# Kernel tuning notes

Measured on AMD Instinct MI355X. Metric: run time of the kernel, lower is better.

The kernel has to match this reference:

```python
import jax, jax.numpy as jnp
import numpy as np
import math

B, L, H, D, S, R = 2, 1024, 8, 64, 10, 128


def setup_inputs() -> dict:
    key = jax.random.key(0)
    k1, k2, k3, k4, k5, k6 = jax.random.split(key, 6)
    return {
        "queries": jax.random.normal(k1, (B, L, H, D), jnp.float32),
        "keys": jax.random.normal(k2, (B, L, H, D), jnp.float32),
        "freqs": jax.random.normal(k3, (H, D, S), jnp.float32),
        "offsets": jax.random.normal(k4, (H, D, S), jnp.float32),
        "gains": jax.random.normal(k5, (H, D, S), jnp.float32),
        "z": jax.random.normal(k6, (B, H, D, 2 * S, R), jnp.float32),
    }


def reference(queries, keys, freqs, offsets, gains, z):
    length = queries.shape[1]
    idx = jnp.arange(length, dtype=queries.dtype)  # [L]
    fr = jax.nn.sigmoid(freqs) / 2.0  # [H,D,S]
    two_pi = 2.0 * math.pi
    # phases: [H,D,L,S]
    phases_q = two_pi * fr[:, :, None, :] * idx[None, None, :, None] + offsets[:, :, None, :]
    phases_k = two_pi * fr[:, :, None, :] * idx[None, None, :, None]
    # interleave cos/sin along last dim -> [H,D,L,2S]
    omega_q = jnp.stack([jnp.cos(phases_q), jnp.sin(phases_q)], axis=-1).reshape(
        phases_q.shape[0], phases_q.shape[1], length, 2 * phases_q.shape[-1])
    omega_k = jnp.stack([jnp.cos(phases_k), jnp.sin(phases_k)], axis=-1).reshape(
        phases_k.shape[0], phases_k.shape[1], length, 2 * phases_k.shape[-1])
    # gains: softplus then repeat(1,1,2) -> concat copies along last dim [H,D,2S]
    g = jax.nn.softplus(gains)
    g2 = jnp.concatenate([g, g], axis=-1)
    scale = 1.0 / math.sqrt(z.shape[-1] * queries.shape[-1])  # 1/sqrt(R*D)
    zs = z * (g2[None, :, :, :, None] * scale)  # [B,H,D,2S,R]
    # fused: qbar[b,h,d,l,r] = sum_s omega_q[h,d,l,s] * zs[b,h,d,s,r];
    # qhat[b,l,h,r] = sum_d qbar[b,l,h,d,r] * queries[b,l,h,d]
    qhat = jnp.einsum('hdls,bhdsr,blhd->blhr', omega_q, zs, queries)
    khat = jnp.einsum('hdls,bhdsr,blhd->blhr', omega_k, zs, keys)
    return (qhat, khat)
```

## Files before the change

### kernel.cpp

```cpp
#include <hip/hip_runtime.h>
#include <math.h>


typedef short bf16x8 __attribute__((ext_vector_type(8)));
typedef float f32x16 __attribute__((ext_vector_type(16)));

__device__ __forceinline__ unsigned int rnd_bf16(float x) {
    union { float f; unsigned int u; } v; v.f = x;
    return v.u + 0x8000u;
}
__device__ __forceinline__ unsigned int pack_bf16(float c, float s) {
    return __builtin_amdgcn_perm(rnd_bf16(s), rnd_bf16(c), 0x07060302u);
}

__global__ __launch_bounds__(256) void prep_z(
    const float* __restrict__ freqs, const float* __restrict__ offsets,
    const float* __restrict__ gains, const float* __restrict__ z,
    uint4* __restrict__ zt, float2* __restrict__ frof)
{
    const float scale = 0.011048543456039806f;
    int bid = blockIdx.x;
    int bh = bid / 20, kb = bid - bh * 20;
    int h = bh & 7;
    int dh = (kb >= 10) ? 1 : 0, s = kb - dh * 10;
    int t = threadIdx.x;

    __shared__ float gsl[64];

    if (t < 16) {
        int i = bid * 16 + t;
        int hh = i / 640, rem = i - hh * 640;
        int ss = rem >> 6, dd = rem & 63;
        int src = (hh * 64 + dd) * 10 + ss;
        float fr = 0.5f / (1.0f + __expf(-freqs[src]));
        frof[i] = make_float2(fr, offsets[src] * 0.15915494309189535f);
        frof[5120 + i] = make_float2(fr, 0.0f);
    }
    if (t < 64) {
        int dl = t >> 1, par = t & 1;
        int tt = 2 * s + par;
        int jm = (tt < 10) ? tt : tt - 10;
        float gn = gains[(h * 64 + dh * 32 + dl) * 10 + jm];
        gsl[t] = (fmaxf(gn, 0.0f) + log1pf(__expf(-fabsf(gn)))) * scale;
    }
    __syncthreads();

    const float* zb = z + (size_t)bh * 163840;
    uint4* outb = zt + (size_t)bid * 1024;

    #pragma unroll
    for (int i = 0; i < 4; i++) {
        int e = i * 256 + t;
        int r = (e >> 1) & 127, c8 = e & 1;
        int dl0 = i * 8 + c8 * 4;
        unsigned int u[4];
        #pragma unroll
        for (int m = 0; m < 4; m++) {
            int dl = dl0 + m;
            int d = dh * 32 + dl;
            float ve = zb[((size_t)d * 20 + 2 * s) * 128 + r] * gsl[dl * 2];
            float vo = zb[((size_t)d * 20 + 2 * s + 1) * 128 + r] * gsl[dl * 2 + 1];
            u[m] = pack_bf16(ve, vo);
        }
        outb[e] = make_uint4(u[0], u[1], u[2], u[3]);
    }
}

__global__ __launch_bounds__(256, 4) void spe_gemm(
    const float* __restrict__ queries, const float* __restrict__ keys,
    const float2* __restrict__ frof, const unsigned short* __restrict__ zt,
    float* __restrict__ out)
{
    __shared__ unsigned int At[2][1024];

    int bid = blockIdx.x;
    int h = bid & 7;
    int u = bid >> 3;
    int qk = u & 1, b = (u >> 1) & 1, lt = u >> 2;
    int l0 = lt * 32;

    int t = threadIdx.x, w = t >> 6, lane = t & 63;
    int ml = lane & 31, hi = lane >> 5;
    int arow = t >> 3, pg = t & 7;

    const float* qsrc = (qk ? keys : queries)
                      + ((size_t)(b * 1024 + l0 + arow) * 8 + h) * 64 + pg * 4;
    const float2* fob = frof + qk * 5120 + h * 640 + pg * 4;
    const unsigned short* bbase = zt + (size_t)(b * 8 + h) * 163840
                                + (w * 32 + ml) * 16 + hi * 8;
    float lf = (float)(l0 + arow);
    unsigned int awz = arow * 32 + ((pg ^ (arow & 7)) << 2);

    float4 qf = *(const float4*)(qsrc);

    bf16x8 n0 = *(const bf16x8*)(bbase);
    bf16x8 n1 = *(const bf16x8*)(bbase + 2048);
    bf16x8 n2 = *(const bf16x8*)(bbase + 4096);
    bf16x8 n3 = *(const bf16x8*)(bbase + 6144);
    {
        const float4* fp = (const float4*)(fob);
        float4 fA = fp[0], fB = fp[1];
        float p0 = __builtin_amdgcn_fractf(fmaf(fA.x, lf, fA.y));
        float p1 = __builtin_amdgcn_fractf(fmaf(fA.z, lf, fA.w));
        float p2 = __builtin_amdgcn_fractf(fmaf(fB.x, lf, fB.y));
        float p3 = __builtin_amdgcn_fractf(fmaf(fB.z, lf, fB.w));
        uint4 a4;
        a4.x = pack_bf16(__builtin_amdgcn_cosf(p0) * qf.x, __builtin_amdgcn_sinf(p0) * qf.x);
        a4.y = pack_bf16(__builtin_amdgcn_cosf(p1) * qf.y, __builtin_amdgcn_sinf(p1) * qf.y);
        a4.z = pack_bf16(__builtin_amdgcn_cosf(p2) * qf.z, __builtin_amdgcn_sinf(p2) * qf.z);
        a4.w = pack_bf16(__builtin_amdgcn_cosf(p3) * qf.w, __builtin_amdgcn_sinf(p3) * qf.w);
        *(uint4*)&At[0][awz] = a4;
    }

    f32x16 acc = {};

    #pragma unroll 2
    for (int kb = 0; kb < 20; kb++) {
        __syncthreads();
        int cur = kb & 1;

        bf16x8 c0 = n0, c1 = n1, c2 = n2, c3 = n3;

        int kn = (kb < 19) ? kb + 1 : 19;
        const unsigned short* tp = bbase + (size_t)kn * 8192;
        n0 = *(const bf16x8*)(tp);
        n1 = *(const bf16x8*)(tp + 2048);
        n2 = *(const bf16x8*)(tp + 4096);
        n3 = *(const bf16x8*)(tp + 6144);

        {
            int dh = (kn >= 10) ? 1 : 0;
            int s = kn - dh * 10;
            if (kn == 10) qf = *(const float4*)(qsrc + 32);
            const float4* fp = (const float4*)(fob + s * 64 + dh * 32);
            float4 fA = fp[0], fB = fp[1];
            float p0 = __builtin_amdgcn_fractf(fmaf(fA.x, lf, fA.y));
            float p1 = __builtin_amdgcn_fractf(fmaf(fA.z, lf, fA.w));
            float p2 = __builtin_amdgcn_fractf(fmaf(fB.x, lf, fB.y));
            float p3 = __builtin_amdgcn_fractf(fmaf(fB.z, lf, fB.w));
            uint4 a4;
            a4.x = pack_bf16(__builtin_amdgcn_cosf(p0) * qf.x, __builtin_amdgcn_sinf(p0) * qf.x);
            a4.y = pack_bf16(__builtin_amdgcn_cosf(p1) * qf.y, __builtin_amdgcn_sinf(p1) * qf.y);
            a4.z = pack_bf16(__builtin_amdgcn_cosf(p2) * qf.z, __builtin_amdgcn_sinf(p2) * qf.z);
            a4.w = pack_bf16(__builtin_amdgcn_cosf(p3) * qf.w, __builtin_amdgcn_sinf(p3) * qf.w);
            *(uint4*)&At[cur ^ 1][awz] = a4;
        }

        #pragma unroll
        for (int ks = 0; ks < 4; ks++) {
            bf16x8 a = *(const bf16x8*)&At[cur][ml * 32 + (((ks * 2 + hi) ^ (ml & 7)) << 2)];
            bf16x8 bb = (ks == 0) ? c0 : (ks == 1) ? c1 : (ks == 2) ? c2 : c3;
            acc = __builtin_amdgcn_mfma_f32_32x32x16_bf16(a, bb, acc, 0, 0, 0);
        }
    }

    float* ob = out + (size_t)qk * 2097152 + (size_t)b * 1048576
              + (size_t)h * 128 + w * 32 + ml;
    #pragma unroll
    for (int reg = 0; reg < 16; reg++) {
        int row = l0 + (reg & 3) + 8 * (reg >> 2) + 4 * hi;
        ob[(size_t)row * 1024] = acc[reg];
    }
}

extern "C" void kernel_launch(void* const* d_in, const int* in_sizes, int n_in,
                              void* d_out, int out_size, void* d_ws, size_t ws_size,
                              hipStream_t stream) {
    const float* queries = (const float*)d_in[0];
    const float* keys    = (const float*)d_in[1];
    const float* freqs   = (const float*)d_in[2];
    const float* offsets = (const float*)d_in[3];
    const float* gains   = (const float*)d_in[4];
    const float* z       = (const float*)d_in[5];
    float* out = (float*)d_out;

    float2* frof = (float2*)d_ws;
    uint4* zt = (uint4*)((char*)d_ws + 81920);

    prep_z<<<320, 256, 0, stream>>>(freqs, offsets, gains, z, zt, frof);
    spe_gemm<<<1024, 256, 0, stream>>>(queries, keys, frof,
                                       (const unsigned short*)zt, out);
}
```

Before: 100.6 us.

## Fuse query and key GEMMs per block to share B-operand loads

Each block now computes both the query and key outputs for the same (b,h,l-tile), so the bf16 z tiles loaded from global memory feed two MFMA accumulators instead of one. The phase product freq*l is shared between the query and key phase computations, and the separate key frequency table is dropped. The grid is halved, each block uses twice the LDS and accumulator registers, and launch bounds drop to 2 blocks per SM, which lowers occupancy and the latency hiding it gives.

```diff
diff --git a/kernel.cpp b/kernel.cpp
--- a/kernel.cpp
+++ b/kernel.cpp
@@ -34,7 +34,6 @@
         int src = (hh * 64 + dd) * 10 + ss;
         float fr = 0.5f / (1.0f + __expf(-freqs[src]));
         frof[i] = make_float2(fr, offsets[src] * 0.15915494309189535f);
-        frof[5120 + i] = make_float2(fr, 0.0f);
     }
     if (t < 64) {
         int dl = t >> 1, par = t & 1;
@@ -66,32 +65,33 @@
     }
 }
 
-__global__ __launch_bounds__(256, 4) void spe_gemm(
+__global__ __launch_bounds__(256, 2) void spe_gemm(
     const float* __restrict__ queries, const float* __restrict__ keys,
     const float2* __restrict__ frof, const unsigned short* __restrict__ zt,
     float* __restrict__ out)
 {
-    __shared__ unsigned int At[2][1024];
+    __shared__ unsigned int At[2][2][1024];
 
     int bid = blockIdx.x;
     int h = bid & 7;
     int u = bid >> 3;
-    int qk = u & 1, b = (u >> 1) & 1, lt = u >> 2;
+    int b = u & 1, lt = u >> 1;
     int l0 = lt * 32;
 
     int t = threadIdx.x, w = t >> 6, lane = t & 63;
     int ml = lane & 31, hi = lane >> 5;
     int arow = t >> 3, pg = t & 7;
 
-    const float* qsrc = (qk ? keys : queries)
-                      + ((size_t)(b * 1024 + l0 + arow) * 8 + h) * 64 + pg * 4;
-    const float2* fob = frof + qk * 5120 + h * 640 + pg * 4;
+    const float* qsrc = queries + ((size_t)(b * 1024 + l0 + arow) * 8 + h) * 64 + pg * 4;
+    const float* ksrc = keys    + ((size_t)(b * 1024 + l0 + arow) * 8 + h) * 64 + pg * 4;
+    const float2* fob = frof + h * 640 + pg * 4;
     const unsigned short* bbase = zt + (size_t)(b * 8 + h) * 163840
                                 + (w * 32 + ml) * 16 + hi * 8;
     float lf = (float)(l0 + arow);
     unsigned int awz = arow * 32 + ((pg ^ (arow & 7)) << 2);
 
     float4 qf = *(const float4*)(qsrc);
+    float4 kf = *(const float4*)(ksrc);
 
     bf16x8 n0 = *(const bf16x8*)(bbase);
     bf16x8 n1 = *(const bf16x8*)(bbase + 2048);
@@ -100,19 +100,30 @@
     {
         const float4* fp = (const float4*)(fob);
         float4 fA = fp[0], fB = fp[1];
-        float p0 = __builtin_amdgcn_fractf(fmaf(fA.x, lf, fA.y));
-        float p1 = __builtin_amdgcn_fractf(fmaf(fA.z, lf, fA.w));
-        float p2 = __builtin_amdgcn_fractf(fmaf(fB.x, lf, fB.y));
-        float p3 = __builtin_amdgcn_fractf(fmaf(fB.z, lf, fB.w));
-        uint4 a4;
-        a4.x = pack_bf16(__builtin_amdgcn_cosf(p0) * qf.x, __builtin_amdgcn_sinf(p0) * qf.x);
-        a4.y = pack_bf16(__builtin_amdgcn_cosf(p1) * qf.y, __builtin_amdgcn_sinf(p1) * qf.y);
-        a4.z = pack_bf16(__builtin_amdgcn_cosf(p2) * qf.z, __builtin_amdgcn_sinf(p2) * qf.z);
-        a4.w = pack_bf16(__builtin_amdgcn_cosf(p3) * qf.w, __builtin_amdgcn_sinf(p3) * qf.w);
-        *(uint4*)&At[0][awz] = a4;
-    }
-
-    f32x16 acc = {};
+        float a0 = fA.x * lf, a1 = fA.z * lf, a2 = fB.x * lf, a3 = fB.z * lf;
+        float pq0 = __builtin_amdgcn_fractf(a0 + fA.y);
+        float pq1 = __builtin_amdgcn_fractf(a1 + fA.w);
+        float pq2 = __builtin_amdgcn_fractf(a2 + fB.y);
+        float pq3 = __builtin_amdgcn_fractf(a3 + fB.w);
+        float pk0 = __builtin_amdgcn_fractf(a0);
+        float pk1 = __builtin_amdgcn_fractf(a1);
+        float pk2 = __builtin_amdgcn_fractf(a2);
+        float pk3 = __builtin_amdgcn_fractf(a3);
+        uint4 aq, ak;
+        aq.x = pack_bf16(__builtin_amdgcn_cosf(pq0) * qf.x, __builtin_amdgcn_sinf(pq0) * qf.x);
+        aq.y = pack_bf16(__builtin_amdgcn_cosf(pq1) * qf.y, __builtin_amdgcn_sinf(pq1) * qf.y);
+        aq.z = pack_bf16(__builtin_amdgcn_cosf(pq2) * qf.z, __builtin_amdgcn_sinf(pq2) * qf.z);
+        aq.w = pack_bf16(__builtin_amdgcn_cosf(pq3) * qf.w, __builtin_amdgcn_sinf(pq3) * qf.w);
+        ak.x = pack_bf16(__builtin_amdgcn_cosf(pk0) * kf.x, __builtin_amdgcn_sinf(pk0) * kf.x);
+        ak.y = pack_bf16(__builtin_amdgcn_cosf(pk1) * kf.y, __builtin_amdgcn_sinf(pk1) * kf.y);
+        ak.z = pack_bf16(__builtin_amdgcn_cosf(pk2) * kf.z, __builtin_amdgcn_sinf(pk2) * kf.z);
+        ak.w = pack_bf16(__builtin_amdgcn_cosf(pk3) * kf.w, __builtin_amdgcn_sinf(pk3) * kf.w);
+        *(uint4*)&At[0][0][awz] = aq;
+        *(uint4*)&At[1][0][awz] = ak;
+    }
+
+    f32x16 accq = {};
+    f32x16 acck = {};
 
     #pragma unroll 2
     for (int kb = 0; kb < 20; kb++) {
@@ -131,35 +142,52 @@
         {
             int dh = (kn >= 10) ? 1 : 0;
             int s = kn - dh * 10;
-            if (kn == 10) qf = *(const float4*)(qsrc + 32);
+            if (kn == 10) {
+                qf = *(const float4*)(qsrc + 32);
+                kf = *(const float4*)(ksrc + 32);
+            }
             const float4* fp = (const float4*)(fob + s * 64 + dh * 32);
             float4 fA = fp[0], fB = fp[1];
-            float p0 = __builtin_amdgcn_fractf(fmaf(fA.x, lf, fA.y));
-            float p1 = __builtin_amdgcn_fractf(fmaf(fA.z, lf, fA.w));
-            float p2 = __builtin_amdgcn_fractf(fmaf(fB.x, lf, fB.y));
-            float p3 = __builtin_amdgcn_fractf(fmaf(fB.z, lf, fB.w));
-            uint4 a4;
-            a4.x = pack_bf16(__builtin_amdgcn_cosf(p0) * qf.x, __builtin_amdgcn_sinf(p0) * qf.x);
-            a4.y = pack_bf16(__builtin_amdgcn_cosf(p1) * qf.y, __builtin_amdgcn_sinf(p1) * qf.y);
-            a4.z = pack_bf16(__builtin_amdgcn_cosf(p2) * qf.z, __builtin_amdgcn_sinf(p2) * qf.z);
-            a4.w = pack_bf16(__builtin_amdgcn_cosf(p3) * qf.w, __builtin_amdgcn_sinf(p3) * qf.w);
-            *(uint4*)&At[cur ^ 1][awz] = a4;
+            float a0 = fA.x * lf, a1 = fA.z * lf, a2 = fB.x * lf, a3 = fB.z * lf;
+            float pq0 = __builtin_amdgcn_fractf(a0 + fA.y);
+            float pq1 = __builtin_amdgcn_fractf(a1 + fA.w);
+            float pq2 = __builtin_amdgcn_fractf(a2 + fB.y);
+            float pq3 = __builtin_amdgcn_fractf(a3 + fB.w);
+            float pk0 = __builtin_amdgcn_fractf(a0);
+            float pk1 = __builtin_amdgcn_fractf(a1);
+            float pk2 = __builtin_amdgcn_fractf(a2);
+            float pk3 = __builtin_amdgcn_fractf(a3);
+            uint4 aq, ak;
+            aq.x = pack_bf16(__builtin_amdgcn_cosf(pq0) * qf.x, __builtin_amdgcn_sinf(pq0) * qf.x);
+            aq.y = pack_bf16(__builtin_amdgcn_cosf(pq1) * qf.y, __builtin_amdgcn_sinf(pq1) * qf.y);
+            aq.z = pack_bf16(__builtin_amdgcn_cosf(pq2) * qf.z, __builtin_amdgcn_sinf(pq2) * qf.z);
+            aq.w = pack_bf16(__builtin_amdgcn_cosf(pq3) * qf.w, __builtin_amdgcn_sinf(pq3) * qf.w);
+            ak.x = pack_bf16(__builtin_amdgcn_cosf(pk0) * kf.x, __builtin_amdgcn_sinf(pk0) * kf.x);
+            ak.y = pack_bf16(__builtin_amdgcn_cosf(pk1) * kf.y, __builtin_amdgcn_sinf(pk1) * kf.y);
+            ak.z = pack_bf16(__builtin_amdgcn_cosf(pk2) * kf.z, __builtin_amdgcn_sinf(pk2) * kf.z);
+            ak.w = pack_bf16(__builtin_amdgcn_cosf(pk3) * kf.w, __builtin_amdgcn_sinf(pk3) * kf.w);
+            *(uint4*)&At[0][cur ^ 1][awz] = aq;
+            *(uint4*)&At[1][cur ^ 1][awz] = ak;
         }
 
         #pragma unroll
         for (int ks = 0; ks < 4; ks++) {
-            bf16x8 a = *(const bf16x8*)&At[cur][ml * 32 + (((ks * 2 + hi) ^ (ml & 7)) << 2)];
+            unsigned int off = ml * 32 + (((ks * 2 + hi) ^ (ml & 7)) << 2);
+            bf16x8 aq = *(const bf16x8*)&At[0][cur][off];
+            bf16x8 ak = *(const bf16x8*)&At[1][cur][off];
             bf16x8 bb = (ks == 0) ? c0 : (ks == 1) ? c1 : (ks == 2) ? c2 : c3;
-            acc = __builtin_amdgcn_mfma_f32_32x32x16_bf16(a, bb, acc, 0, 0, 0);
+            accq = __builtin_amdgcn_mfma_f32_32x32x16_bf16(aq, bb, accq, 0, 0, 0);
+            acck = __builtin_amdgcn_mfma_f32_32x32x16_bf16(ak, bb, acck, 0, 0, 0);
         }
     }
 
-    float* ob = out + (size_t)qk * 2097152 + (size_t)b * 1048576
-              + (size_t)h * 128 + w * 32 + ml;
+    float* obq = out + (size_t)b * 1048576 + (size_t)h * 128 + w * 32 + ml;
+    float* obk = obq + 2097152;
     #pragma unroll
     for (int reg = 0; reg < 16; reg++) {
         int row = l0 + (reg & 3) + 8 * (reg >> 2) + 4 * hi;
-        ob[(size_t)row * 1024] = acc[reg];
+        obq[(size_t)row * 1024] = accq[reg];
+        obk[(size_t)row * 1024] = acck[reg];
     }
 }
 
@@ -178,6 +206,6 @@
     uint4* zt = (uint4*)((char*)d_ws + 81920);
 
     prep_z<<<320, 256, 0, stream>>>(freqs, offsets, gains, z, zt, frof);
-    spe_gemm<<<1024, 256, 0, stream>>>(queries, keys, frof,
-                                       (const unsigned short*)zt, out);
-}
+    spe_gemm<<<512, 256, 0, stream>>>(queries, keys, frof,
+                                      (const unsigned short*)zt, out);
+}
```

New measurement: 99.44 us, median of 2. About the same (-1.2%).
